# Kernel tuning notes

Hardware: AMD Instinct MI355X
Metric: run time of the kernel (lower is better)

## Reference

```python
import jax, jax.numpy as jnp
import numpy as np

N = 1_000_000
NG = 128                 # n_grid
DX = 1.0 / NG
DT = 1e-4
P_VOL = (DX * 0.5) ** 2
P_RHO = 1.0
GRAVITY = 9.8
HID = 16


def setup_inputs() -> dict:
    key = jax.random.key(0)
    ks = jax.random.split(key, 14)
    x = 0.1 + 0.8 * jax.random.uniform(ks[0], (N, 2), dtype=jnp.float32)
    v = 0.1 * jax.random.normal(ks[1], (N, 2), dtype=jnp.float32)
    C = 0.01 * jax.random.normal(ks[2], (N, 2, 2), dtype=jnp.float32)
    F = jnp.eye(2, dtype=jnp.float32)[None] + 0.01 * jax.random.normal(ks[3], (N, 2, 2), dtype=jnp.float32)
    material = jax.random.randint(ks[4], (N,), 0, 3, dtype=jnp.int32)
    Jp = jnp.ones((N, 1), dtype=jnp.float32)
    E = jnp.full((1,), 1000.0, dtype=jnp.float32)
    nu = jnp.full((1,), 0.2, dtype=jnp.float32)
    # PsiModel2d MLP params: Linear(2,16) -> Linear(16,16) -> Linear(16,16) -> Linear(16,1)
    s = 0.3
    W1 = s * jax.random.normal(ks[5], (HID, 2), dtype=jnp.float32)
    b1 = jnp.zeros((HID,), dtype=jnp.float32)
    W2 = s * jax.random.normal(ks[6], (HID, HID), dtype=jnp.float32)
    b2 = jnp.zeros((HID,), dtype=jnp.float32)
    W3 = s * jax.random.normal(ks[7], (HID, HID), dtype=jnp.float32)
    b3 = jnp.zeros((HID,), dtype=jnp.float32)
    W4 = s * jax.random.normal(ks[8], (1, HID), dtype=jnp.float32)
    b4 = jnp.zeros((1,), dtype=jnp.float32)
    return dict(x=x, v=v, C=C, F=F, material=material, Jp=Jp, E=E, nu=nu,
                W1=W1, b1=b1, W2=W2, b2=b2, W3=W3, b3=b3, W4=W4, b4=b4)


def _psi_sum(F, W1, b1, W2, b2, W3, b3, W4, b4):
    # PsiModel2d, input_type='eigen': Psi(sigma_1, sigma_2) of C = F^T F
    Cm = jnp.einsum('nki,nkj->nij', F, F)
    tr_C = Cm[:, 0, 0] + Cm[:, 1, 1]
    det_C = Cm[:, 0, 0] * Cm[:, 1, 1] - Cm[:, 0, 1] * Cm[:, 1, 0]
    delta = jnp.sqrt(jnp.maximum(tr_C ** 2 - 4.0 * det_C, 1e-8))
    feat = jnp.stack([0.5 * (tr_C + delta), 0.5 * (tr_C - delta)], axis=1)  # [N,2]
    h = jax.nn.relu(feat @ W1.T + b1)
    h = jax.nn.relu(h @ W2.T + b2)
    h = jax.nn.relu(h @ W3.T + b3)
    return (h @ W4.T + b4).sum()


def reference(x, v, C, F, material, Jp, E, nu, W1, b1, W2, b2, W3, b3, W4, b4):
    inv_dx = float(NG)
    p_mass = P_VOL * P_RHO
    n = x.shape[0]

    base = jnp.floor(x * inv_dx - 0.5).astype(jnp.int32)   # [N,2]
    fx = x * inv_dx - base.astype(x.dtype)                  # [N,2]
    # quadratic B-spline weights, [3,N,2]
    w = jnp.stack([0.5 * (1.5 - fx) ** 2,
                   0.75 - (fx - 1.0) ** 2,
                   0.5 * (fx - 0.5) ** 2], axis=0)

    F_new = F + DT * jnp.einsum('nij,njk->nik', C, F)
    # stress = d(sum Psi)/dF  (learned energy)
    stress = jax.grad(_psi_sum)(F_new, W1, b1, W2, b2, W3, b3, W4, b4)
    stress = (-DT * P_VOL * 4.0 * inv_dx ** 2) * stress
    affine = stress + p_mass * C                            # [N,2,2]

    v_add = p_mass * v - jnp.einsum('nij,nj->ni', affine, x)  # [N,2]
    vals = jnp.concatenate([v_add, affine.reshape(n, 4),
                            jnp.full((n, 1), p_mass, x.dtype)], axis=1)  # [N,7]

    # P2G: scatter-add over 3x3 stencil into flattened grid
    grid = jnp.zeros((NG * NG, 7), x.dtype)
    for i in range(3):
        for j in range(3):
            wt = w[i, :, 0] * w[j, :, 1]                    # [N]
            idx = (base[:, 0] + i) * NG + (base[:, 1] + j)  # [N]
            grid = grid.at[idx].add(wt[:, None] * vals)
    grid = grid.reshape(NG, NG, 7)
    grid_v = grid[..., :2]
    grid_affine = grid[..., 2:6].reshape(NG, NG, 2, 2)
    grid_m = grid[..., 6]

    gx = jnp.stack(jnp.meshgrid(jnp.arange(NG), jnp.arange(NG), indexing='ij'),
                   axis=-1).astype(x.dtype) * DX            # [NG,NG,2]
    grid_v = grid_v + jnp.einsum('xyij,xyj->xyi', grid_affine, gx)
    nonempty = grid_m > 0
    grid_v = jnp.where(nonempty[..., None],
                       grid_v / jnp.where(nonempty, grid_m, 1.0)[..., None],
                       grid_v)
    grid_v = grid_v.at[:, :, 1].add(-DT * GRAVITY)
    # boundary conditions
    grid_v = grid_v.at[:3, :, 0].set(jnp.maximum(grid_v[:3, :, 0], 0.0))
    grid_v = grid_v.at[-3:, :, 0].set(jnp.minimum(grid_v[-3:, :, 0], 0.0))
    grid_v = grid_v.at[:, :3, 1].set(jnp.maximum(grid_v[:, :3, 1], 0.0))
    grid_v = grid_v.at[:, -3:, 1].set(jnp.minimum(grid_v[:, -3:, 1], 0.0))

    # G2P: gather v and v (x) grid_x outer product over 3x3 stencil
    grid_C = grid_v[..., :, None] * gx[..., None, :]        # [NG,NG,2,2]
    gvals = jnp.concatenate([grid_v, grid_C.reshape(NG, NG, 4)], axis=-1)  # [NG,NG,6]
    acc = jnp.zeros((n, 6), x.dtype)
    for i in range(3):
        for j in range(3):
            wt = w[i, :, 0] * w[j, :, 1]
            acc = acc + wt[:, None] * gvals[base[:, 0] + i, base[:, 1] + j]
    new_v = acc[:, :2]
    new_C = acc[:, 2:].reshape(n, 2, 2)
    new_C = (4.0 * inv_dx ** 2) * (new_C - new_v[:, :, None] * x[:, None, :])

    return (x + DT * v, new_v, new_C, F_new, material, Jp)
```

## Files before the change

kernel.cpp:

```cpp
#include <hip/hip_runtime.h>
#include <math.h>

constexpr int   NGc    = 128;
constexpr int   NCELL  = NGc * NGc;
constexpr int   NBIN   = 128 * 32;
constexpr float DTc    = 1e-4f;
constexpr float DXc    = 1.0f / 128.0f;
constexpr float INV_DX = 128.0f;
constexpr float P_VOLc = (DXc * 0.5f) * (DXc * 0.5f);
constexpr float P_MASSc = P_VOLc * 1.0f;
constexpr float GRAV   = 9.8f;
constexpr float STRESS_COEF = -DTc * P_VOLc * 4.0f * INV_DX * INV_DX;

constexpr int S1_PPT = 16;
constexpr int S1_BLK = 1024;

__global__ __launch_bounds__(1024) void bin_kernel(
    const float2* __restrict__ x, unsigned* __restrict__ key,
    unsigned* __restrict__ gcnt, int n)
{
    __shared__ unsigned hist[NBIN];
#pragma unroll
    for (int j = 0; j < NBIN / S1_BLK; j++)
        hist[threadIdx.x + j * S1_BLK] = 0;
    __syncthreads();

    int base_i = blockIdx.x * (S1_BLK * S1_PPT);
    unsigned t_arr[S1_PPT], r_arr[S1_PPT];
#pragma unroll
    for (int k = 0; k < S1_PPT; k++) {
        int i = base_i + k * S1_BLK + threadIdx.x;
        unsigned t = 0, r = 0;
        if (i < n) {
            float2 xi = x[i];
            int bx = (int)floorf(xi.x * INV_DX - 0.5f);
            int by = (int)floorf(xi.y * INV_DX - 0.5f);
            t = (unsigned)(bx * 32 + (by >> 2));
            r = atomicAdd(&hist[t], 1u);
        }
        t_arr[k] = t; r_arr[k] = r;
    }
    __syncthreads();

#pragma unroll
    for (int j = 0; j < NBIN / S1_BLK; j++) {
        int b = threadIdx.x + j * S1_BLK;
        unsigned c = hist[b];
        __syncthreads();
        hist[b] = c ? atomicAdd(&gcnt[b], c) : 0u;
        __syncthreads();
    }

#pragma unroll
    for (int k = 0; k < S1_PPT; k++) {
        int i = base_i + k * S1_BLK + threadIdx.x;
        if (i < n)
            key[i] = (t_arr[k] << 20) | (hist[t_arr[k]] + r_arr[k]);
    }
}

__global__ __launch_bounds__(1024) void scan_kernel(
    const unsigned* __restrict__ gcnt, unsigned* __restrict__ binoff)
{
    __shared__ unsigned s[1024];
    int t = threadIdx.x;
    unsigned v0 = gcnt[4 * t], v1 = gcnt[4 * t + 1];
    unsigned v2 = gcnt[4 * t + 2], v3 = gcnt[4 * t + 3];
    unsigned p = v0 + v1 + v2 + v3;
    s[t] = p;
    __syncthreads();
    for (int d = 1; d < 1024; d <<= 1) {
        unsigned add = (t >= d) ? s[t - d] : 0u;
        __syncthreads();
        s[t] += add;
        __syncthreads();
    }
    unsigned base = s[t] - p;
    binoff[4 * t]     = base;
    binoff[4 * t + 1] = base + v0;
    binoff[4 * t + 2] = base + v0 + v1;
    binoff[4 * t + 3] = base + v0 + v1 + v2;
    if (t == 1023) binoff[4096] = s[1023];
}

__global__ __launch_bounds__(256) void stagea_kernel(
    const float2* __restrict__ x, const float2* __restrict__ v,
    const float4* __restrict__ C, const float4* __restrict__ F,
    const float* __restrict__ W1, const float* __restrict__ b1,
    const float* __restrict__ W2, const float* __restrict__ b2,
    const float* __restrict__ W3, const float* __restrict__ b3,
    const float* __restrict__ W4,
    const unsigned* __restrict__ key, const unsigned* __restrict__ binoff,
    float4* __restrict__ recs, int n)
{
    int i = blockIdx.x * 256 + threadIdx.x;
    if (i >= n) return;

    float2 xi = x[i];
    float2 vi = v[i];
    float4 Ci = C[i];
    float4 Fi = F[i];

    float Fn00 = Fi.x + DTc * (Ci.x * Fi.x + Ci.y * Fi.z);
    float Fn01 = Fi.y + DTc * (Ci.x * Fi.y + Ci.y * Fi.w);
    float Fn10 = Fi.z + DTc * (Ci.z * Fi.x + Ci.w * Fi.z);
    float Fn11 = Fi.w + DTc * (Ci.z * Fi.y + Ci.w * Fi.w);

    float Cm00 = Fn00 * Fn00 + Fn10 * Fn10;
    float Cm01 = Fn00 * Fn01 + Fn10 * Fn11;
    float Cm11 = Fn01 * Fn01 + Fn11 * Fn11;

    float tr  = Cm00 + Cm11;
    float det = Cm00 * Cm11 - Cm01 * Cm01;
    float g   = tr * tr - 4.0f * det;
    float gate = (g > 1e-8f) ? 1.0f : 0.0f;
    float delta = sqrtf(fmaxf(g, 1e-8f));
    float feat0 = 0.5f * (tr + delta);
    float feat1 = 0.5f * (tr - delta);

    float h1[16], h2[16], h3[16];
#pragma unroll
    for (int j = 0; j < 16; j++)
        h1[j] = fmaxf(W1[2 * j] * feat0 + W1[2 * j + 1] * feat1 + b1[j], 0.0f);
#pragma unroll
    for (int j = 0; j < 16; j++) {
        float a = b2[j];
#pragma unroll
        for (int kk = 0; kk < 16; kk++) a += W2[j * 16 + kk] * h1[kk];
        h2[j] = fmaxf(a, 0.0f);
    }
#pragma unroll
    for (int j = 0; j < 16; j++) {
        float a = b3[j];
#pragma unroll
        for (int kk = 0; kk < 16; kk++) a += W3[j * 16 + kk] * h2[kk];
        h3[j] = fmaxf(a, 0.0f);
    }

    float dh3[16];
#pragma unroll
    for (int j = 0; j < 16; j++) dh3[j] = (h3[j] > 0.0f) ? W4[j] : 0.0f;

    float dh2[16];
#pragma unroll
    for (int kk = 0; kk < 16; kk++) {
        float a = 0.0f;
#pragma unroll
        for (int j = 0; j < 16; j++) a += W3[j * 16 + kk] * dh3[j];
        dh2[kk] = (h2[kk] > 0.0f) ? a : 0.0f;
    }

    float dfeat0 = 0.0f, dfeat1 = 0.0f;
#pragma unroll
    for (int kk = 0; kk < 16; kk++) {
        float a = 0.0f;
#pragma unroll
        for (int j = 0; j < 16; j++) a += W2[j * 16 + kk] * dh2[j];
        float dh1k = (h1[kk] > 0.0f) ? a : 0.0f;
        dfeat0 += W1[2 * kk] * dh1k;
        dfeat1 += W1[2 * kk + 1] * dh1k;
    }

    float half_sum  = 0.5f * (dfeat0 + dfeat1);
    float half_diff = 0.5f * (dfeat0 - dfeat1);
    float inv_delta = 1.0f / delta;
    float dtr  = half_sum + half_diff * tr * inv_delta * gate;
    float ddet = half_diff * (-2.0f) * inv_delta * gate;

    float S00 = 2.0f * (dtr + ddet * Cm11);
    float S11 = 2.0f * (dtr + ddet * Cm00);
    float S01 = -2.0f * ddet * Cm01;

    float dF00 = Fn00 * S00 + Fn01 * S01;
    float dF01 = Fn00 * S01 + Fn01 * S11;
    float dF10 = Fn10 * S00 + Fn11 * S01;
    float dF11 = Fn10 * S01 + Fn11 * S11;

    float a00 = STRESS_COEF * dF00 + P_MASSc * Ci.x;
    float a01 = STRESS_COEF * dF01 + P_MASSc * Ci.y;
    float a10 = STRESS_COEF * dF10 + P_MASSc * Ci.z;
    float a11 = STRESS_COEF * dF11 + P_MASSc * Ci.w;

    unsigned k = key[i];
    unsigned pos = binoff[k >> 20] + (k & 0xFFFFFu);

    recs[2 * (size_t)pos]     = make_float4(xi.x, xi.y, a00, a01);
    recs[2 * (size_t)pos + 1] = make_float4(a10, a11, P_MASSc * vi.x, P_MASSc * vi.y);
}

__global__ __launch_bounds__(256) void grid_gather_kernel(
    const float4* __restrict__ recs, const unsigned* __restrict__ binoff,
    float2* __restrict__ gv)
{
    int wid  = threadIdx.x >> 6;
    int lane = threadIdx.x & 63;
    int node = blockIdx.x * 4 + wid;
    int gi = node >> 7;
    int gj = node & 127;

    const float gxx = (float)gi * DXc;
    const float gxy = (float)gj * DXc;

    float accx = 0.0f, accy = 0.0f, accm = 0.0f;

    int c0 = max(gj - 2, 0) >> 2;
    int c1 = min(gj, 127) >> 2;

#pragma unroll
    for (int r = 0; r < 3; r++) {
        int bx = gi - 2 + r;
        if (bx < 0 || bx > 127) continue;
        int lo = (int)binoff[bx * 32 + c0];
        int hi = (int)binoff[bx * 32 + c1 + 1];
        for (int k = lo + lane; k < hi; k += 64) {
            float4 r0 = recs[2 * (size_t)k];
            float4 r1 = recs[2 * (size_t)k + 1];

            float py = r0.y * INV_DX;
            int   by = (int)floorf(py - 0.5f);
            int   jj = gj - by;
            bool  ok = (jj >= 0) && (jj <= 2);

            float fy = py - (float)by;
            float fx = r0.x * INV_DX - (float)bx;

            float wx;
            if (r == 0)      wx = 0.5f * (fx - 0.5f) * (fx - 0.5f);
            else if (r == 1) wx = 0.75f - (fx - 1.0f) * (fx - 1.0f);
            else             wx = 0.5f * (1.5f - fx) * (1.5f - fx);

            float wy0 = 0.5f * (1.5f - fy) * (1.5f - fy);
            float wy1 = 0.75f - (fy - 1.0f) * (fy - 1.0f);
            float wy2 = 0.5f * (fy - 0.5f) * (fy - 0.5f);
            float wy = (jj == 0) ? wy0 : ((jj == 1) ? wy1 : wy2);

            float wt = ok ? (wx * wy) : 0.0f;
            float dxp = gxx - r0.x;
            float dyp = gxy - r0.y;
            accx += wt * (r1.z + r0.z * dxp + r0.w * dyp);
            accy += wt * (r1.w + r1.x * dxp + r1.y * dyp);
            accm += wt * P_MASSc;
        }
    }

#pragma unroll
    for (int off = 32; off >= 1; off >>= 1) {
        accx += __shfl_xor(accx, off, 64);
        accy += __shfl_xor(accy, off, 64);
        accm += __shfl_xor(accm, off, 64);
    }

    if (lane == 0) {
        float vx = accx, vy = accy;
        if (accm > 0.0f) {
            float inv_m = 1.0f / accm;
            vx *= inv_m;
            vy *= inv_m;
        }
        vy -= DTc * GRAV;
        if (gi < 3)        vx = fmaxf(vx, 0.0f);
        if (gi >= NGc - 3) vx = fminf(vx, 0.0f);
        if (gj < 3)        vy = fmaxf(vy, 0.0f);
        if (gj >= NGc - 3) vy = fminf(vy, 0.0f);
        gv[node] = make_float2(vx, vy);
    }
}

__global__ __launch_bounds__(256) void g2p_kernel(
    const float2* __restrict__ x, const float2* __restrict__ v,
    const float4* __restrict__ C, const float4* __restrict__ F,
    const int* __restrict__ material, const float* __restrict__ Jp,
    const float2* __restrict__ gv,
    float2* __restrict__ out_x, float2* __restrict__ out_v,
    float4* __restrict__ out_C, float4* __restrict__ out_F,
    float* __restrict__ out_mat, float* __restrict__ out_Jp, int n)
{
    int i = blockIdx.x * 256 + threadIdx.x;
    if (i >= n) return;

    float2 xi = x[i];
    float2 vi = v[i];
    float4 Ci = C[i];
    float4 Fi = F[i];

    float Fn00 = Fi.x + DTc * (Ci.x * Fi.x + Ci.y * Fi.z);
    float Fn01 = Fi.y + DTc * (Ci.x * Fi.y + Ci.y * Fi.w);
    float Fn10 = Fi.z + DTc * (Ci.z * Fi.x + Ci.w * Fi.z);
    float Fn11 = Fi.w + DTc * (Ci.z * Fi.y + Ci.w * Fi.w);

    float px = xi.x * INV_DX, py = xi.y * INV_DX;
    int   bx = (int)floorf(px - 0.5f);
    int   by = (int)floorf(py - 0.5f);
    float fx = px - (float)bx;
    float fy = py - (float)by;
    float wxs[3] = {0.5f * (1.5f - fx) * (1.5f - fx),
                    0.75f - (fx - 1.0f) * (fx - 1.0f),
                    0.5f * (fx - 0.5f) * (fx - 0.5f)};
    float wys[3] = {0.5f * (1.5f - fy) * (1.5f - fy),
                    0.75f - (fy - 1.0f) * (fy - 1.0f),
                    0.5f * (fy - 0.5f) * (fy - 0.5f)};

    float accvx = 0.0f, accvy = 0.0f;
    float accC00 = 0.0f, accC01 = 0.0f, accC10 = 0.0f, accC11 = 0.0f;

#pragma unroll
    for (int ii = 0; ii < 3; ii++) {
        float gxx = (float)(bx + ii) * DXc;
#pragma unroll
        for (int jj = 0; jj < 3; jj++) {
            float wt = wxs[ii] * wys[jj];
            float2 gvn = gv[(bx + ii) * NGc + (by + jj)];
            float gxy = (float)(by + jj) * DXc;
            accvx  += wt * gvn.x;
            accvy  += wt * gvn.y;
            accC00 += wt * gvn.x * gxx;
            accC01 += wt * gvn.x * gxy;
            accC10 += wt * gvn.y * gxx;
            accC11 += wt * gvn.y * gxy;
        }
    }

    const float k4 = 4.0f * INV_DX * INV_DX;
    out_x[i]   = make_float2(xi.x + DTc * vi.x, xi.y + DTc * vi.y);
    out_v[i]   = make_float2(accvx, accvy);
    out_C[i]   = make_float4(k4 * (accC00 - accvx * xi.x),
                             k4 * (accC01 - accvx * xi.y),
                             k4 * (accC10 - accvy * xi.x),
                             k4 * (accC11 - accvy * xi.y));
    out_F[i]   = make_float4(Fn00, Fn01, Fn10, Fn11);
    out_mat[i] = (float)material[i];
    out_Jp[i]  = Jp[i];
}

extern "C" void kernel_launch(void* const* d_in, const int* in_sizes, int n_in,
                              void* d_out, int out_size, void* d_ws, size_t ws_size,
                              hipStream_t stream)
{
    const float2* x  = (const float2*)d_in[0];
    const float2* v  = (const float2*)d_in[1];
    const float4* C  = (const float4*)d_in[2];
    const float4* F  = (const float4*)d_in[3];
    const int* material = (const int*)d_in[4];
    const float* Jp  = (const float*)d_in[5];
    const float* W1  = (const float*)d_in[8];
    const float* b1  = (const float*)d_in[9];
    const float* W2  = (const float*)d_in[10];
    const float* b2  = (const float*)d_in[11];
    const float* W3  = (const float*)d_in[12];
    const float* b3  = (const float*)d_in[13];
    const float* W4  = (const float*)d_in[14];

    const int n = in_sizes[0] / 2;

    unsigned* gcnt   = (unsigned*)d_ws;
    unsigned* binoff = gcnt + NBIN;
    float2*   gv     = (float2*)(binoff + NBIN + 1);

    float* out = (float*)d_out;
    float2* out_x   = (float2*)out;
    float2* out_v   = (float2*)(out + 2 * (size_t)n);
    float4* out_C   = (float4*)(out + 4 * (size_t)n);
    float4* out_F   = (float4*)(out + 8 * (size_t)n);
    float*  out_mat = out + 12 * (size_t)n;
    float*  out_Jp  = out + 13 * (size_t)n;

    float4*   recs = (float4*)(out + 2 * (size_t)n);
    unsigned* key  = (unsigned*)out_mat;

    hipMemsetAsync(gcnt, 0, NBIN * sizeof(unsigned), stream);

    int s1_blocks = (n + S1_BLK * S1_PPT - 1) / (S1_BLK * S1_PPT);
    int blocks    = (n + 255) / 256;
    bin_kernel<<<s1_blocks, S1_BLK, 0, stream>>>(x, key, gcnt, n);
    scan_kernel<<<1, 1024, 0, stream>>>(gcnt, binoff);
    stagea_kernel<<<blocks, 256, 0, stream>>>(x, v, C, F, W1, b1, W2, b2, W3, b3, W4,
                                              key, binoff, recs, n);
    grid_gather_kernel<<<NCELL / 4, 256, 0, stream>>>(recs, binoff, gv);
    g2p_kernel<<<blocks, 256, 0, stream>>>(x, v, C, F, material, Jp, gv,
                                           out_x, out_v, out_C, out_F, out_mat, out_Jp, n);
}
```

Before: 297.1 us.

## Gather 8 grid nodes per wavefront with per-lane LDS scatter accumulators

The grid gather kernel now gives each wavefront 8 consecutive grid nodes in a column instead of one. Each particle record is read once and scattered into up to 3 of the 8 nodes through per-lane LDS slices, which are then reduced across lanes. This cuts redundant record reads, since the old version re-read every particle for each of its 3 y-neighbour nodes. It adds LDS atomics, LDS zeroing and a 64-way serial reduction per node. The stagea kernel also gets an occupancy hint in its launch bounds.

Measured after the change: 465.8 us. +56.8%, slower.

```diff
diff --git a/kernel.cpp b/kernel.cpp
--- a/kernel.cpp
+++ b/kernel.cpp
@@ -83,7 +83,7 @@
     if (t == 1023) binoff[4096] = s[1023];
 }
 
-__global__ __launch_bounds__(256) void stagea_kernel(
+__global__ __launch_bounds__(256, 2) void stagea_kernel(
     const float2* __restrict__ x, const float2* __restrict__ v,
     const float4* __restrict__ C, const float4* __restrict__ F,
     const float* __restrict__ W1, const float* __restrict__ b1,
@@ -192,19 +192,21 @@
     const float4* __restrict__ recs, const unsigned* __restrict__ binoff,
     float2* __restrict__ gv)
 {
+    __shared__ float lds[4 * 64 * 25];
+
     int wid  = threadIdx.x >> 6;
     int lane = threadIdx.x & 63;
-    int node = blockIdx.x * 4 + wid;
-    int gi = node >> 7;
-    int gj = node & 127;
-
-    const float gxx = (float)gi * DXc;
-    const float gxy = (float)gj * DXc;
-
-    float accx = 0.0f, accy = 0.0f, accm = 0.0f;
-
-    int c0 = max(gj - 2, 0) >> 2;
-    int c1 = min(gj, 127) >> 2;
+    int w    = blockIdx.x * 4 + wid;
+    int base = w * 8;
+    int gi   = base >> 7;
+    int gj0  = base & 127;
+
+    float* slice = lds + (wid * 64 + lane) * 25;
+#pragma unroll
+    for (int t = 0; t < 25; t++) slice[t] = 0.0f;
+
+    int c0 = max(gj0 - 2, 0) >> 2;
+    int c1 = (gj0 + 7) >> 2;
 
 #pragma unroll
     for (int r = 0; r < 3; r++) {
@@ -218,9 +220,6 @@
 
             float py = r0.y * INV_DX;
             int   by = (int)floorf(py - 0.5f);
-            int   jj = gj - by;
-            bool  ok = (jj >= 0) && (jj <= 2);
-
             float fy = py - (float)by;
             float fx = r0.x * INV_DX - (float)bx;
 
@@ -229,31 +228,41 @@
             else if (r == 1) wx = 0.75f - (fx - 1.0f) * (fx - 1.0f);
             else             wx = 0.5f * (1.5f - fx) * (1.5f - fx);
 
-            float wy0 = 0.5f * (1.5f - fy) * (1.5f - fy);
-            float wy1 = 0.75f - (fy - 1.0f) * (fy - 1.0f);
-            float wy2 = 0.5f * (fy - 0.5f) * (fy - 0.5f);
-            float wy = (jj == 0) ? wy0 : ((jj == 1) ? wy1 : wy2);
-
-            float wt = ok ? (wx * wy) : 0.0f;
-            float dxp = gxx - r0.x;
-            float dyp = gxy - r0.y;
-            accx += wt * (r1.z + r0.z * dxp + r0.w * dyp);
-            accy += wt * (r1.w + r1.x * dxp + r1.y * dyp);
-            accm += wt * P_MASSc;
+            float wys[3] = {0.5f * (1.5f - fy) * (1.5f - fy),
+                            0.75f - (fy - 1.0f) * (fy - 1.0f),
+                            0.5f * (fy - 0.5f) * (fy - 0.5f)};
+
+            float dxp = (float)gi * DXc - r0.x;
+#pragma unroll
+            for (int jj = 0; jj < 3; jj++) {
+                int gjn = by + jj;
+                int t   = gjn - gj0;
+                if (t >= 0 && t < 8) {
+                    float wt  = wx * wys[jj];
+                    float dyp = (float)gjn * DXc - r0.y;
+                    atomicAdd(slice + t * 3 + 0, wt * (r1.z + r0.z * dxp + r0.w * dyp));
+                    atomicAdd(slice + t * 3 + 1, wt * (r1.w + r1.x * dxp + r1.y * dyp));
+                    atomicAdd(slice + t * 3 + 2, wt * P_MASSc);
+                }
+            }
         }
     }
-
-#pragma unroll
-    for (int off = 32; off >= 1; off >>= 1) {
-        accx += __shfl_xor(accx, off, 64);
-        accy += __shfl_xor(accy, off, 64);
-        accm += __shfl_xor(accm, off, 64);
-    }
-
-    if (lane == 0) {
-        float vx = accx, vy = accy;
-        if (accm > 0.0f) {
-            float inv_m = 1.0f / accm;
+    __syncthreads();
+
+    float tot = 0.0f;
+    if (lane < 24) {
+        const float* wbase = lds + wid * 64 * 25;
+        for (int i2 = 0; i2 < 64; i2++) tot += wbase[i2 * 25 + lane];
+    }
+
+    float vx = __shfl(tot, 3 * lane,     64);
+    float vy = __shfl(tot, 3 * lane + 1, 64);
+    float m  = __shfl(tot, 3 * lane + 2, 64);
+
+    if (lane < 8) {
+        int gj = gj0 + lane;
+        if (m > 0.0f) {
+            float inv_m = 1.0f / m;
             vx *= inv_m;
             vy *= inv_m;
         }
@@ -262,7 +271,7 @@
         if (gi >= NGc - 3) vx = fminf(vx, 0.0f);
         if (gj < 3)        vy = fmaxf(vy, 0.0f);
         if (gj >= NGc - 3) vy = fminf(vy, 0.0f);
-        gv[node] = make_float2(vx, vy);
+        gv[base + lane] = make_float2(vx, vy);
     }
 }
 
@@ -375,7 +384,7 @@
     scan_kernel<<<1, 1024, 0, stream>>>(gcnt, binoff);
     stagea_kernel<<<blocks, 256, 0, stream>>>(x, v, C, F, W1, b1, W2, b2, W3, b3, W4,
                                               key, binoff, recs, n);
-    grid_gather_kernel<<<NCELL / 4, 256, 0, stream>>>(recs, binoff, gv);
+    grid_gather_kernel<<<NCELL / 8 / 4, 256, 0, stream>>>(recs, binoff, gv);
     g2p_kernel<<<blocks, 256, 0, stream>>>(x, v, C, F, material, Jp, gv,
                                            out_x, out_v, out_C, out_F, out_mat, out_Jp, n);
 }
```
